# Performance work log

Hardware: AMD Instinct MI355X
Metric: run time of the kernel (lower is better)

The kernel has to match this reference:

```python
import jax, jax.numpy as jnp
import numpy as np
import math

B, T, C, H, D, R = 1, 2048, 2048, 16, 128, 64
W_LOCAL = 512
DELTA_I = 0.75
ROPE_BASE = 10000.0


def _rotate(x):
    # interleaved rotate-half, exactly as in the torch source
    x1, x2 = x[..., ::2], x[..., 1::2]
    return jnp.stack((-x2, x1), axis=-1).reshape(x.shape)


def _rope_tables(seq_len):
    inv_freq = 1.0 / (ROPE_BASE ** (jnp.arange(0, D, 2, dtype=jnp.float32) / D))
    t = jnp.arange(seq_len, dtype=jnp.float32)
    freqs = jnp.einsum('i,j->ij', t, inv_freq)          # [T, D/2]
    emb = jnp.concatenate((freqs, freqs), axis=-1)      # [T, D] (half-layout, as in source)
    return jnp.cos(emb)[None, None], jnp.sin(emb)[None, None]


def setup_inputs() -> dict:
    key = jax.random.key(0)
    ks = jax.random.split(key, 8)
    s = 0.02
    return {
        'x': jax.random.normal(ks[0], (B, T, C), dtype=jnp.float32),
        'w_qkv': jax.random.normal(ks[1], (3 * C, C), dtype=jnp.float32) * s,
        'w_o': jax.random.normal(ks[2], (C, C), dtype=jnp.float32) * s,
        'pk': jax.random.normal(ks[3], (R, D), dtype=jnp.float32) * s,
        'pv': jax.random.normal(ks[4], (R, D), dtype=jnp.float32) * s,
        'uo': jax.random.normal(ks[5], (D, R), dtype=jnp.float32) * s,
        'info_w1': jax.random.normal(ks[6], (C // 4, C), dtype=jnp.float32) * s,
        'info_w2': jax.random.normal(ks[7], (1, C // 4), dtype=jnp.float32) * s,
    }


def reference(x, w_qkv, w_o, pk, pv, uo, info_w1, info_w2):
    Bx, Tx, Cx = x.shape
    scale = 1.0 / math.sqrt(D)

    qkv = x @ w_qkv.T                                   # [B,T,3C]
    q, k, v = jnp.split(qkv, 3, axis=-1)
    q = q.reshape(Bx, Tx, H, D).transpose(0, 2, 1, 3)   # [B,H,T,D]
    k = k.reshape(Bx, Tx, H, D).transpose(0, 2, 1, 3)
    v = v.reshape(Bx, Tx, H, D).transpose(0, 2, 1, 3)

    cos, sin = _rope_tables(Tx)
    q = q * cos + _rotate(q) * sin
    k = k * cos + _rotate(k) * sin

    # causal local-window attention (full [B,H,T,T] scores, as in source)
    w = min(W_LOCAL, Tx)
    idx = jnp.arange(Tx)
    rel = idx[None, :] - idx[:, None]                   # j - i
    local_mask = (rel > 0) | (rel < -(w - 1))           # True = masked
    scores = jnp.einsum('bhtd,bhsd->bhts', q, k) * scale
    scores = jnp.where(local_mask[None, None], -jnp.inf, scores)
    attn_local = jax.nn.softmax(scores, axis=-1)
    ctx_local = jnp.einsum('bhts,bhsd->bhtd', attn_local, v)

    # informational gate (no-grad path in source)
    h_info = jax.nn.gelu(x @ info_w1.T, approximate=False)
    info_score = jax.nn.sigmoid((h_info @ info_w2.T)[..., 0])   # [B,T]
    gate = (info_score > DELTA_I).astype(x.dtype)

    # low-rank global path (unmasked softmax over all tokens, as in source)
    k_r = jnp.einsum('bhsd,rd->bhsr', k, pk)
    v_r = jnp.einsum('bhsd,rd->bhsr', v, pv)
    q_r = jnp.einsum('bhtd,rd->bhtr', q, pk)
    scores_g = jnp.einsum('bhtr,bhsr->bhts', q_r, k_r) * (scale * D / R)
    attn_g = jax.nn.softmax(scores_g, axis=-1)
    ctx_g_r = jnp.einsum('bhts,bhsr->bhtr', attn_g, v_r)
    ctx_g = jnp.einsum('bhtr,dr->bhtd', ctx_g_r, uo)
    gate_q = gate[:, None, :, None]                     # [B,1,T,1]
    ctx = ctx_local + ctx_g * gate_q

    ctx = ctx.transpose(0, 2, 1, 3).reshape(Bx, Tx, Cx)
    return ctx @ w_o.T
```

## Files before the change

kernel.cpp:

```cpp
#include <hip/hip_runtime.h>
#include <hip/hip_bf16.h>
#include <math.h>

#define T_LEN 2048
#define C_DIM 2048
#define NH 16
#define HD 128
#define RANK 64
#define W_LOCAL 512
#define QKV_LD 6144
#define ROW_BF 12288
#define KB_OFF 4096
#define VB_OFF 8192
#define WO_OFF 6144
#define SCALE 0.08838834764831845f
#define SCALE_G 0.17677669529663687f
#define LOG1E4_OVER_64 0.14391156831212787f

typedef __bf16 bf16_t;
typedef __bf16 bf16x8 __attribute__((ext_vector_type(8)));
typedef __bf16 bf16x4 __attribute__((ext_vector_type(4)));
typedef float f32x4 __attribute__((ext_vector_type(4)));

__device__ __forceinline__ void async_copy16(const bf16_t* g, bf16_t* l) {
    __builtin_amdgcn_global_load_lds(
        (const __attribute__((address_space(1))) unsigned int*)g,
        (__attribute__((address_space(3))) unsigned int*)l, 16, 0, 0);
}

__global__ __launch_bounds__(256)
void prep_kernel(const float* __restrict__ x, bf16_t* __restrict__ xb,
                 bf16_t* __restrict__ xlo,
                 const float* __restrict__ w1, bf16_t* __restrict__ w1hi,
                 bf16_t* __restrict__ w1lo,
                 const float* __restrict__ w_qkv, bf16_t* __restrict__ wqb,
                 float* __restrict__ tab) {
    const int bid = blockIdx.x;
    const int tid = threadIdx.x;
    if (bid < 2560) {
        const float* in;
        bf16_t *hi, *lo;
        int idx;
        if (bid < 2048) { in = x; hi = xb; lo = xlo; idx = bid * 256 + tid; }
        else            { in = w1; hi = w1hi; lo = w1lo; idx = (bid - 2048) * 256 + tid; }
        const float* p = in + (size_t)idx * 8;
        float4 v0 = *(const float4*)p;
        float4 v1 = *(const float4*)(p + 4);
        float v[8] = {v0.x, v0.y, v0.z, v0.w, v1.x, v1.y, v1.z, v1.w};
        bf16x8 h, l;
#pragma unroll
        for (int i = 0; i < 8; ++i) {
            bf16_t hb = (bf16_t)v[i];
            h[i] = hb;
            l[i] = (bf16_t)(v[i] - (float)hb);
        }
        *(bf16x8*)(hi + (size_t)idx * 8) = h;
        *(bf16x8*)(lo + (size_t)idx * 8) = l;
    } else if (bid < 8704) {
        int idx = (bid - 2560) * 256 + tid;
        const float* p = w_qkv + (size_t)idx * 8;
        float4 v0 = *(const float4*)p;
        float4 v1 = *(const float4*)(p + 4);
        bf16x8 o;
        o[0] = (bf16_t)v0.x; o[1] = (bf16_t)v0.y; o[2] = (bf16_t)v0.z; o[3] = (bf16_t)v0.w;
        o[4] = (bf16_t)v1.x; o[5] = (bf16_t)v1.y; o[6] = (bf16_t)v1.z; o[7] = (bf16_t)v1.w;
        *(bf16x8*)(wqb + (size_t)idx * 8) = o;
    } else {
        int idx = (bid - 8704) * 256 + tid;
        int t = idx >> 6, j = idx & 63;
        float inv = expf(-(float)j * LOG1E4_OVER_64);
        float s, c;
        sincosf((float)t * inv, &s, &c);
        tab[t * 128 + j] = c;
        tab[t * 128 + 64 + j] = s;
    }
}

#define NTK 32

#define STG_A(bb, ktile) do {                                                  \
    _Pragma("unroll")                                                          \
    for (int c_ = 0; c_ < 4; ++c_)                                             \
        async_copy16(gA + (size_t)(c_ * 32) * 2048 + (ktile) * 64,             \
                     &lds[bb][0][(c_ * 32 + rS) * 64 + dS]);                   \
} while (0)

#define STG_B(bb, ktile) do {                                                  \
    _Pragma("unroll")                                                          \
    for (int c_ = 0; c_ < 4; ++c_)                                             \
        async_copy16(gB + (size_t)(c_ * 32) * 2048 + (ktile) * 64,             \
                     &lds[bb][1][(c_ * 32 + rS) * 64 + dS]);                   \
} while (0)

#define RD_A(bb, m, k) (*(const bf16x8*)&lds[bb][0][(wr * 64 + (m) * 16 + l16) * 64 + (((k) * 4 + quad) ^ xsw) * 8])
#define RD_B(bb, n, k) (*(const bf16x8*)&lds[bb][1][(wc * 64 + (n) * 16 + l16) * 64 + (((k) * 4 + quad) ^ xsw) * 8])

__global__ __launch_bounds__(256, 2)
void gemm_qkv_rope(const bf16_t* __restrict__ A, const bf16_t* __restrict__ B,
                   float* __restrict__ qkv, bf16_t* __restrict__ qkv_bf,
                   const float* __restrict__ tab, const float* __restrict__ w_o) {
    const int bid = blockIdx.x;
    const int tid = threadIdx.x;
    if (bid >= 768) {
        int row = bid - 768;
        int c = tid * 8;
        const float* p = w_o + (size_t)row * 2048 + c;
        float4 v0 = *(const float4*)p;
        float4 v1 = *(const float4*)(p + 4);
        bf16x8 o;
        o[0] = (bf16_t)v0.x; o[1] = (bf16_t)v0.y; o[2] = (bf16_t)v0.z; o[3] = (bf16_t)v0.w;
        o[4] = (bf16_t)v1.x; o[5] = (bf16_t)v1.y; o[6] = (bf16_t)v1.z; o[7] = (bf16_t)v1.w;
        *(bf16x8*)(qkv_bf + (size_t)row * ROW_BF + WO_OFF + c) = o;
        return;
    }

    __shared__ __align__(16) bf16_t lds[2][2][128 * 64];

    const int xcd = bid & 7, idx = bid >> 3;
    const int bn_ = xcd * 6 + (idx >> 4);
    const int bm_ = idx & 15;
    const int wave = tid >> 6, lane = tid & 63;
    const int quad = lane >> 4, l16 = lane & 15;
    const int wr = wave >> 1, wc = wave & 1;
    const int xsw = l16 & 7;

    const int rS = tid >> 3;
    const int cS = ((tid & 7) ^ (rS & 7)) * 8;
    const int dS = (tid & 7) * 8;
    const bf16_t* gA = A + (size_t)(bm_ * 128 + rS) * 2048 + cS;
    const bf16_t* gB = B + (size_t)(bn_ * 128 + rS) * 2048 + cS;

    f32x4 acc[4][4];
#pragma unroll
    for (int i = 0; i < 4; ++i)
#pragma unroll
        for (int j = 0; j < 4; ++j) acc[i][j] = (f32x4){0.f, 0.f, 0.f, 0.f};

    STG_A(0, 0); STG_B(0, 0);
    STG_A(1, 1); STG_B(1, 1);
    asm volatile("s_waitcnt vmcnt(8)" ::: "memory");
    __builtin_amdgcn_s_barrier();

    for (int kt = 0; kt < NTK; ++kt) {
        const int b = kt & 1;
        bf16x8 af[4][2], bfr[4][2];
#pragma unroll
        for (int m = 0; m < 4; ++m) { af[m][0] = RD_A(b, m, 0); af[m][1] = RD_A(b, m, 1); }
#pragma unroll
        for (int n = 0; n < 4; ++n) { bfr[n][0] = RD_B(b, n, 0); bfr[n][1] = RD_B(b, n, 1); }
        asm volatile("s_waitcnt lgkmcnt(0)" ::: "memory");
        __builtin_amdgcn_s_barrier();

        __builtin_amdgcn_s_setprio(1);
#pragma unroll
        for (int m = 0; m < 4; ++m)
#pragma unroll
            for (int n = 0; n < 4; ++n)
                acc[m][n] = __builtin_amdgcn_mfma_f32_16x16x32_bf16(af[m][0], bfr[n][0], acc[m][n], 0, 0, 0);
        __builtin_amdgcn_s_setprio(0);
        if (kt + 2 < NTK) STG_A(b, kt + 2);

        __builtin_amdgcn_s_setprio(1);
#pragma unroll
        for (int m = 0; m < 4; ++m)
#pragma unroll
            for (int n = 0; n < 4; ++n)
                acc[m][n] = __builtin_amdgcn_mfma_f32_16x16x32_bf16(af[m][1], bfr[n][1], acc[m][n], 0, 0, 0);
        __builtin_amdgcn_s_setprio(0);
        if (kt + 2 < NTK) STG_B(b, kt + 2);

        if (kt < NTK - 2) { asm volatile("s_waitcnt vmcnt(8)" ::: "memory"); }
        else              { asm volatile("s_waitcnt vmcnt(0)" ::: "memory"); }
        __builtin_amdgcn_s_barrier();
    }

    const int colbase = bn_ * 128 + wc * 64;
    const int region = colbase >> 11;
    const int rowbase = bm_ * 128 + wr * 64;
    const bool odd = (l16 & 1);

    if (region == 2) {
#pragma unroll
        for (int mt = 0; mt < 4; ++mt)
#pragma unroll
            for (int r = 0; r < 4; ++r) {
                int t = rowbase + mt * 16 + quad * 4 + r;
                bf16_t* brow = qkv_bf + (size_t)t * ROW_BF + VB_OFF + (colbase - 4096);
#pragma unroll
                for (int nt = 0; nt < 4; ++nt)
                    brow[nt * 16 + l16] = (bf16_t)acc[mt][nt][r];
            }
    } else {
#pragma unroll
        for (int mt = 0; mt < 4; ++mt)
#pragma unroll
            for (int r = 0; r < 4; ++r) {
                int t = rowbase + mt * 16 + quad * 4 + r;
                const float* trow = tab + t * 128;
#pragma unroll
                for (int nt = 0; nt < 4; ++nt) {
                    float v = acc[mt][nt][r];
                    float vp = __shfl_xor(v, 1);
                    int col = colbase + nt * 16 + l16;
                    int j = col & 63;
                    float c = trow[j], s = trow[64 + j];
                    float y = odd ? (v * c + vp * s) : (v * c - vp * s);
                    if (region == 0)
                        qkv[(size_t)t * QKV_LD + col] = y;
                    else
                        qkv_bf[(size_t)t * ROW_BF + KB_OFF + (col - 2048)] = (bf16_t)y;
                }
            }
    }
}

#define STG_A2(bb, ktile) do {                                                 \
    _Pragma("unroll")                                                          \
    for (int c_ = 0; c_ < 4; ++c_)                                             \
        async_copy16(gA + (size_t)(c_ * 32) * 2048 + (ktile) * 64,             \
                     &lds[bb][0][(c_ * 32 + rS) * 64 + dS]);                   \
} while (0)

#define STG_B2(bb, ktile) do {                                                 \
    _Pragma("unroll")                                                          \
    for (int c_ = 0; c_ < 4; ++c_)                                             \
        async_copy16(gB + (size_t)(c_ * 32) * ROW_BF + (ktile) * 64,           \
                     &lds[bb][1][(c_ * 32 + rS) * 64 + dS]);                   \
} while (0)

__global__ __launch_bounds__(256, 2)
void gemm_ctx_wo(const bf16_t* __restrict__ A, const bf16_t* __restrict__ Bov,
                 float* __restrict__ C) {
    __shared__ __align__(16) bf16_t lds[2][2][128 * 64];

    const int bid = blockIdx.x;
    const int xcd = bid & 7, idx = bid >> 3;
    const int bn_ = xcd * 2 + (idx >> 4);
    const int bm_ = idx & 15;
    const int tid = threadIdx.x;
    const int wave = tid >> 6, lane = tid & 63;
    const int quad = lane >> 4, l16 = lane & 15;
    const int wr = wave >> 1, wc = wave & 1;
    const int xsw = l16 & 7;

    const int rS = tid >> 3;
    const int cS = ((tid & 7) ^ (rS & 7)) * 8;
    const int dS = (tid & 7) * 8;
    const bf16_t* gA = A + (size_t)(bm_ * 128 + rS) * 2048 + cS;
    const bf16_t* gB = Bov + (size_t)(bn_ * 128 + rS) * ROW_BF + cS;

    f32x4 acc[4][4];
#pragma unroll
    for (int i = 0; i < 4; ++i)
#pragma unroll
        for (int j = 0; j < 4; ++j) acc[i][j] = (f32x4){0.f, 0.f, 0.f, 0.f};

    STG_A2(0, 0); STG_B2(0, 0);
    STG_A2(1, 1); STG_B2(1, 1);
    asm volatile("s_waitcnt vmcnt(8)" ::: "memory");
    __builtin_amdgcn_s_barrier();

    for (int kt = 0; kt < NTK; ++kt) {
        const int b = kt & 1;
        bf16x8 af[4][2], bfr[4][2];
#pragma unroll
        for (int m = 0; m < 4; ++m) { af[m][0] = RD_A(b, m, 0); af[m][1] = RD_A(b, m, 1); }
#pragma unroll
        for (int n = 0; n < 4; ++n) { bfr[n][0] = RD_B(b, n, 0); bfr[n][1] = RD_B(b, n, 1); }
        asm volatile("s_waitcnt lgkmcnt(0)" ::: "memory");
        __builtin_amdgcn_s_barrier();

        __builtin_amdgcn_s_setprio(1);
#pragma unroll
        for (int m = 0; m < 4; ++m)
#pragma unroll
            for (int n = 0; n < 4; ++n)
                acc[m][n] = __builtin_amdgcn_mfma_f32_16x16x32_bf16(af[m][0], bfr[n][0], acc[m][n], 0, 0, 0);
        __builtin_amdgcn_s_setprio(0);
        if (kt + 2 < NTK) STG_A2(b, kt + 2);

        __builtin_amdgcn_s_setprio(1);
#pragma unroll
        for (int m = 0; m < 4; ++m)
#pragma unroll
            for (int n = 0; n < 4; ++n)
                acc[m][n] = __builtin_amdgcn_mfma_f32_16x16x32_bf16(af[m][1], bfr[n][1], acc[m][n], 0, 0, 0);
        __builtin_amdgcn_s_setprio(0);
        if (kt + 2 < NTK) STG_B2(b, kt + 2);

        if (kt < NTK - 2) { asm volatile("s_waitcnt vmcnt(8)" ::: "memory"); }
        else              { asm volatile("s_waitcnt vmcnt(0)" ::: "memory"); }
        __builtin_amdgcn_s_barrier();
    }

    const int colbase = bn_ * 128 + wc * 64;
    const int rowbase = bm_ * 128 + wr * 64;
#pragma unroll
    for (int mt = 0; mt < 4; ++mt)
#pragma unroll
        for (int r = 0; r < 4; ++r) {
            int row = rowbase + mt * 16 + quad * 4 + r;
            float* crow = C + (size_t)row * 2048 + colbase;
#pragma unroll
            for (int nt = 0; nt < 4; ++nt)
                crow[nt * 16 + l16] = acc[mt][nt][r];
        }
}

#define GBK 32

__global__ __launch_bounds__(256)
void info_gemm_mfma(const bf16_t* __restrict__ Ahi, const bf16_t* __restrict__ Alo,
                    const bf16_t* __restrict__ Bhi, const bf16_t* __restrict__ Blo,
                    float* __restrict__ Cpart) {
    __shared__ bf16_t Ah[128 * GBK];
    __shared__ bf16_t Al[128 * GBK];
    __shared__ bf16_t Bh[128 * GBK];
    __shared__ bf16_t Bl[128 * GBK];
    const int tid = threadIdx.x;
    const int wave = tid >> 6, lane = tid & 63;
    const int quad = lane >> 4, l16 = lane & 15;
    const int bm = blockIdx.y * 128, bn = blockIdx.x * 128;
    const int ks = blockIdx.z;
    const int wm = (wave >> 1) * 64, wn = (wave & 1) * 64;
    const int lrow = lane >> 2;
    const int lkb = (lane & 3) * 8;
    const int kbeg = ks * 512;

    f32x4 acc[4][4];
#pragma unroll
    for (int i = 0; i < 4; ++i)
#pragma unroll
        for (int j = 0; j < 4; ++j) acc[i][j] = (f32x4){0.f, 0.f, 0.f, 0.f};

    const size_t aoff = (size_t)(bm + wave * 16 + lrow) * 2048 + lkb + kbeg;
    const size_t boff = (size_t)(bn + wave * 16 + lrow) * 2048 + lkb + kbeg;
    bf16_t* lAh = &Ah[(wave * 16 + lrow) * GBK + lkb];
    bf16_t* lAl = &Al[(wave * 16 + lrow) * GBK + lkb];
    bf16_t* lBh = &Bh[(wave * 16 + lrow) * GBK + lkb];
    bf16_t* lBl = &Bl[(wave * 16 + lrow) * GBK + lkb];

    for (int k0 = 0; k0 < 512; k0 += GBK) {
        __syncthreads();
        async_copy16(Ahi + aoff + k0, lAh);
        async_copy16(Ahi + aoff + (size_t)64 * 2048 + k0, lAh + 64 * GBK);
        async_copy16(Alo + aoff + k0, lAl);
        async_copy16(Alo + aoff + (size_t)64 * 2048 + k0, lAl + 64 * GBK);
        async_copy16(Bhi + boff + k0, lBh);
        async_copy16(Bhi + boff + (size_t)64 * 2048 + k0, lBh + 64 * GBK);
        async_copy16(Blo + boff + k0, lBl);
        async_copy16(Blo + boff + (size_t)64 * 2048 + k0, lBl + 64 * GBK);
        __syncthreads();

        bf16x8 ah[4], al[4], bh[4], bl[4];
#pragma unroll
        for (int mt = 0; mt < 4; ++mt) {
            ah[mt] = *(const bf16x8*)&Ah[(wm + mt * 16 + l16) * GBK + quad * 8];
            al[mt] = *(const bf16x8*)&Al[(wm + mt * 16 + l16) * GBK + quad * 8];
        }
#pragma unroll
        for (int nt = 0; nt < 4; ++nt) {
            bh[nt] = *(const bf16x8*)&Bh[(wn + nt * 16 + l16) * GBK + quad * 8];
            bl[nt] = *(const bf16x8*)&Bl[(wn + nt * 16 + l16) * GBK + quad * 8];
        }
#pragma unroll
        for (int mt = 0; mt < 4; ++mt)
#pragma unroll
            for (int nt = 0; nt < 4; ++nt) {
                acc[mt][nt] = __builtin_amdgcn_mfma_f32_16x16x32_bf16(ah[mt], bh[nt], acc[mt][nt], 0, 0, 0);
                acc[mt][nt] = __builtin_amdgcn_mfma_f32_16x16x32_bf16(ah[mt], bl[nt], acc[mt][nt], 0, 0, 0);
                acc[mt][nt] = __builtin_amdgcn_mfma_f32_16x16x32_bf16(al[mt], bh[nt], acc[mt][nt], 0, 0, 0);
            }
    }

    float* cp = Cpart + (size_t)ks * 2048 * 512;
#pragma unroll
    for (int mt = 0; mt < 4; ++mt)
#pragma unroll
        for (int r = 0; r < 4; ++r) {
            int row = bm + wm + mt * 16 + quad * 4 + r;
            float* crow = cp + (size_t)row * 512 + bn + wn;
#pragma unroll
            for (int nt = 0; nt < 4; ++nt)
                crow[nt * 16 + l16] = acc[mt][nt][r];
        }
}

__device__ __forceinline__ float gelu_exact(float v) {
    return 0.5f * v * (1.0f + erff(v * 0.70710678118654752f));
}

__global__ __launch_bounds__(64)
void info_gate_kernel(const float* __restrict__ Cpart, const float* __restrict__ w2,
                      float* __restrict__ gate) {
    const int t = blockIdx.x;
    const int lane = threadIdx.x;
    const float* p0 = Cpart + (size_t)t * 512;
    float s = 0.f;
#pragma unroll
    for (int i = lane; i < 512; i += 64) {
        float v = ((p0[i] + p0[i + 1048576]) + p0[i + 2097152]) + p0[i + 3145728];
        s += gelu_exact(v) * w2[i];
    }
#pragma unroll
    for (int off = 32; off > 0; off >>= 1) s += __shfl_down(s, off);
    if (lane == 0) {
        float sig = 1.f / (1.f + expf(-s));
        gate[t] = (sig > 0.75f) ? 1.f : 0.f;
    }
}

#define KV_LD 136

__global__ __launch_bounds__(256)
void kvr_mfma_kernel(const float* __restrict__ qkv, const bf16_t* __restrict__ qkv_bf,
                     const float* __restrict__ pk, const float* __restrict__ pv,
                     float* __restrict__ kr, float* __restrict__ vr,
                     bf16_t* __restrict__ qr) {
    __shared__ bf16_t Kt[64 * KV_LD];
    __shared__ bf16_t Vt[64 * KV_LD];
    __shared__ bf16_t Qt[64 * KV_LD];
    __shared__ bf16_t Pk[64 * KV_LD];
    __shared__ bf16_t Pv[64 * KV_LD];

    const int h = blockIdx.y;
    const int s0 = blockIdx.x * 64;
    const int tid = threadIdx.x;
    const int wave = tid >> 6, lane = tid & 63;
    const int quad = lane >> 4, l16 = lane & 15;

#pragma unroll
    for (int i = 0; i < 4; ++i) {
        int gid = i * 256 + tid;
        int row = gid >> 4, ch = (gid & 15) << 3;
        const bf16_t* rb = qkv_bf + (size_t)(s0 + row) * ROW_BF + h * HD + ch;
        *(bf16x8*)&Kt[row * KV_LD + ch] = *(const bf16x8*)(rb + KB_OFF);
        *(bf16x8*)&Vt[row * KV_LD + ch] = *(const bf16x8*)(rb + VB_OFF);
    }
#pragma unroll
    for (int i = 0; i < 8; ++i) {
        int gid = i * 256 + tid;
        int row = gid >> 5, c = (gid & 31) << 2;
        float4 vq = *(const float4*)(qkv + (size_t)(s0 + row) * QKV_LD + h * HD + c);
        bf16x4 pq;
        pq[0] = (bf16_t)vq.x; pq[1] = (bf16_t)vq.y; pq[2] = (bf16_t)vq.z; pq[3] = (bf16_t)vq.w;
        *(bf16x4*)&Qt[row * KV_LD + c] = pq;
        float4 wk = *(const float4*)(pk + (size_t)row * HD + c);
        float4 wv = *(const float4*)(pv + (size_t)row * HD + c);
        bf16x4 qk4, qv4;
        qk4[0] = (bf16_t)wk.x; qk4[1] = (bf16_t)wk.y; qk4[2] = (bf16_t)wk.z; qk4[3] = (bf16_t)wk.w;
        qv4[0] = (bf16_t)wv.x; qv4[1] = (bf16_t)wv.y; qv4[2] = (bf16_t)wv.z; qv4[3] = (bf16_t)wv.w;
        *(bf16x4*)&Pk[row * KV_LD + c] = qk4;
        *(bf16x4*)&Pv[row * KV_LD + c] = qv4;
    }
    __syncthreads();

    f32x4 ak[4], av[4], aq[4];
#pragma unroll
    for (int nt = 0; nt < 4; ++nt) {
        ak[nt] = (f32x4){0.f, 0.f, 0.f, 0.f};
        av[nt] = (f32x4){0.f, 0.f, 0.f, 0.f};
        aq[nt] = (f32x4){0.f, 0.f, 0.f, 0.f};
    }

#pragma unroll
    for (int ks = 0; ks < 4; ++ks) {
        const int ao = (wave * 16 + l16) * KV_LD + ks * 32 + quad * 8;
        bf16x8 a_k = *(const bf16x8*)&Kt[ao];
        bf16x8 a_v = *(const bf16x8*)&Vt[ao];
        bf16x8 a_q = *(const bf16x8*)&Qt[ao];
#pragma unroll
        for (int nt = 0; nt < 4; ++nt) {
            const int bo = (nt * 16 + l16) * KV_LD + ks * 32 + quad * 8;
            bf16x8 bk = *(const bf16x8*)&Pk[bo];
            bf16x8 bv = *(const bf16x8*)&Pv[bo];
            ak[nt] = __builtin_amdgcn_mfma_f32_16x16x32_bf16(a_k, bk, ak[nt], 0, 0, 0);
            av[nt] = __builtin_amdgcn_mfma_f32_16x16x32_bf16(a_v, bv, av[nt], 0, 0, 0);
            aq[nt] = __builtin_amdgcn_mfma_f32_16x16x32_bf16(a_q, bk, aq[nt], 0, 0, 0);
        }
    }

#pragma unroll
    for (int nt = 0; nt < 4; ++nt)
#pragma unroll
        for (int r = 0; r < 4; ++r) {
            int s = s0 + wave * 16 + quad * 4 + r;
            size_t idx = ((size_t)h * T_LEN + s) * RANK + nt * 16 + l16;
            kr[idx] = ak[nt][r];
            vr[idx] = av[nt][r];
            qr[idx] = (bf16_t)aq[nt][r];
        }
}

#define QTI 64
#define KTI 64
#define QS_LD 136
#define VT_LD 68
#define PS_LD 72

__global__ __launch_bounds__(256)
void local_attn_kernel(const float* __restrict__ qkv, const bf16_t* __restrict__ qkv_bf,
                       bf16_t* __restrict__ cxb) {
    __shared__ bf16_t Qs[QTI * QS_LD];
    __shared__ bf16_t Ks[KTI * HD];
    __shared__ bf16_t Vt[HD * VT_LD];
    __shared__ bf16_t Ps[4][16 * PS_LD];

    const int h = blockIdx.y;
    const int t0 = blockIdx.x * QTI;
    const int tid = threadIdx.x;
    const int wave = tid >> 6, lane = tid & 63;
    const int quad = lane >> 4, l16 = lane & 15;

#pragma unroll
    for (int i = 0; i < 8; ++i) {
        int gid = i * 256 + tid;
        int row = gid >> 5, c4 = (gid & 31) << 2;
        const float4 v = *(const float4*)(qkv + (size_t)(t0 + row) * QKV_LD + h * HD + c4);
        bf16x4 p;
        p[0] = (bf16_t)(v.x * SCALE); p[1] = (bf16_t)(v.y * SCALE);
        p[2] = (bf16_t)(v.z * SCALE); p[3] = (bf16_t)(v.w * SCALE);
        *(bf16x4*)&Qs[row * QS_LD + c4] = p;
    }

    f32x4 o[8];
#pragma unroll
    for (int d8 = 0; d8 < 8; ++d8) o[d8] = (f32x4){0.f, 0.f, 0.f, 0.f};
    float m_i[4] = {-1e30f, -1e30f, -1e30f, -1e30f};
    float l_i[4] = {0.f, 0.f, 0.f, 0.f};

    __syncthreads();

    for (int kt = 0; kt < 9; ++kt) {
        const int sbase = t0 - 512 + kt * KTI;
        if (sbase < 0) continue;
        __syncthreads();
#pragma unroll
        for (int i = 0; i < 4; ++i) {
            int s = i * 256 + tid;
            int row = s >> 4, ch = s & 15;
            int gch = ch ^ (row & 7);
            const bf16_t* src = qkv_bf + (size_t)(sbase + row) * ROW_BF + KB_OFF + h * HD + gch * 8;
            async_copy16(src, &Ks[s * 8]);
        }
#pragma unroll
        for (int i = 0; i < 8; ++i) {
            int gid = i * 256 + tid;
            int row = gid >> 5, c4 = (gid & 31) << 2;
            bf16x4 vv = *(const bf16x4*)(qkv_bf + (size_t)(sbase + row) * ROW_BF + VB_OFF + h * HD + c4);
            Vt[(c4 + 0) * VT_LD + row] = vv[0];
            Vt[(c4 + 1) * VT_LD + row] = vv[1];
            Vt[(c4 + 2) * VT_LD + row] = vv[2];
            Vt[(c4 + 3) * VT_LD + row] = vv[3];
        }
        __syncthreads();

        f32x4 sacc[4];
#pragma unroll
        for (int nt = 0; nt < 4; ++nt) sacc[nt] = (f32x4){0.f, 0.f, 0.f, 0.f};
#pragma unroll
        for (int ks = 0; ks < 4; ++ks) {
            bf16x8 a = *(const bf16x8*)&Qs[(wave * 16 + l16) * QS_LD + ks * 32 + quad * 8];
#pragma unroll
            for (int nt = 0; nt < 4; ++nt) {
                int r = nt * 16 + l16;
                int ch = (ks * 4 + quad) ^ (r & 7);
                bf16x8 b = *(const bf16x8*)&Ks[r * HD + ch * 8];
                sacc[nt] = __builtin_amdgcn_mfma_f32_16x16x32_bf16(a, b, sacc[nt], 0, 0, 0);
            }
        }

        if (kt == 0 || kt == 8) {
#pragma unroll
            for (int nt = 0; nt < 4; ++nt) {
                int s_g = sbase + nt * 16 + l16;
#pragma unroll
                for (int r = 0; r < 4; ++r) {
                    int t_g = t0 + wave * 16 + quad * 4 + r;
                    bool valid = (s_g <= t_g) && (s_g + W_LOCAL > t_g);
                    if (!valid) sacc[nt][r] = -1e30f;
                }
            }
        }

#pragma unroll
        for (int r = 0; r < 4; ++r) {
            float mx = fmaxf(fmaxf(sacc[0][r], sacc[1][r]), fmaxf(sacc[2][r], sacc[3][r]));
            mx = fmaxf(mx, __shfl_xor(mx, 1));
            mx = fmaxf(mx, __shfl_xor(mx, 2));
            mx = fmaxf(mx, __shfl_xor(mx, 4));
            mx = fmaxf(mx, __shfl_xor(mx, 8));
            float mnew = fmaxf(m_i[r], mx);
            float alpha = __expf(m_i[r] - mnew);
            m_i[r] = mnew;
            float rs = 0.f;
#pragma unroll
            for (int nt = 0; nt < 4; ++nt) {
                float p = __expf(sacc[nt][r] - mnew);
                sacc[nt][r] = p;
                rs += p;
            }
            rs += __shfl_xor(rs, 1);
            rs += __shfl_xor(rs, 2);
            rs += __shfl_xor(rs, 4);
            rs += __shfl_xor(rs, 8);
            l_i[r] = l_i[r] * alpha + rs;
#pragma unroll
            for (int d8 = 0; d8 < 8; ++d8) o[d8][r] *= alpha;
        }

#pragma unroll
        for (int r = 0; r < 4; ++r)
#pragma unroll
            for (int nt = 0; nt < 4; ++nt)
                Ps[wave][(quad * 4 + r) * PS_LD + nt * 16 + l16] = (bf16_t)sacc[nt][r];

#pragma unroll
        for (int ks2 = 0; ks2 < 2; ++ks2) {
            bf16x8 a = *(const bf16x8*)&Ps[wave][l16 * PS_LD + ks2 * 32 + quad * 8];
#pragma unroll
            for (int d8 = 0; d8 < 8; ++d8) {
                const bf16_t* vb = &Vt[(d8 * 16 + l16) * VT_LD + ks2 * 32 + quad * 8];
                bf16x4 b0 = *(const bf16x4*)vb;
                bf16x4 b1 = *(const bf16x4*)(vb + 4);
                bf16x8 b;
                b[0] = b0[0]; b[1] = b0[1]; b[2] = b0[2]; b[3] = b0[3];
                b[4] = b1[0]; b[5] = b1[1]; b[6] = b1[2]; b[7] = b1[3];
                o[d8] = __builtin_amdgcn_mfma_f32_16x16x32_bf16(a, b, o[d8], 0, 0, 0);
            }
        }
    }

#pragma unroll
    for (int r = 0; r < 4; ++r) {
        float inv = 1.0f / l_i[r];
        size_t rowoff = (size_t)(t0 + wave * 16 + quad * 4 + r) * 2048 + h * HD;
#pragma unroll
        for (int d8 = 0; d8 < 8; ++d8)
            cxb[rowoff + d8 * 16 + l16] = (bf16_t)(o[d8][r] * inv);
    }
}

__device__ __forceinline__ float block_reduce_max512(float v, float* red, int tid) {
    red[tid] = v; __syncthreads();
    for (int s = 256; s > 0; s >>= 1) {
        if (tid < s) red[tid] = fmaxf(red[tid], red[tid + s]);
        __syncthreads();
    }
    float r = red[0]; __syncthreads();
    return r;
}
__device__ __forceinline__ float block_reduce_sum512(float v, float* red, int tid) {
    red[tid] = v; __syncthreads();
    for (int s = 256; s > 0; s >>= 1) {
        if (tid < s) red[tid] = red[tid] + red[tid + s];
        __syncthreads();
    }
    float r = red[0]; __syncthreads();
    return r;
}

__global__ __launch_bounds__(512)
void global_attn_kernel(bf16_t* __restrict__ cxb, const float* __restrict__ kr,
                        const float* __restrict__ vr, const bf16_t* __restrict__ qr,
                        const float* __restrict__ uo, const float* __restrict__ gate) {
    const int t = blockIdx.x, h = blockIdx.y;
    if (gate[t] <= 0.5f) return;

    __shared__ float qrs[64];
    __shared__ float red[512];
    __shared__ float cgr[64];
    __shared__ float sg[2048];
    const int tid = threadIdx.x;

    if (tid < 64) qrs[tid] = (float)qr[((size_t)h * T_LEN + t) * RANK + tid];
    __syncthreads();

    const float* krh = kr + (size_t)h * T_LEN * RANK;
    const float* vrh = vr + (size_t)h * T_LEN * RANK;
    float lmax = -INFINITY;
    for (int s = tid; s < T_LEN; s += 512) {
        const float* krr = krh + (size_t)s * RANK;
        float acc = 0.f;
#pragma unroll
        for (int r = 0; r < RANK; r += 4) {
            float4 k4 = *(const float4*)(krr + r);
            acc += qrs[r] * k4.x + qrs[r + 1] * k4.y + qrs[r + 2] * k4.z + qrs[r + 3] * k4.w;
        }
        float sc = acc * SCALE_G;
        sg[s] = sc;
        lmax = fmaxf(lmax, sc);
    }
    float gmx = block_reduce_max512(lmax, red, tid);
    float lsum = 0.f;
    for (int s = tid; s < T_LEN; s += 512) {
        float pp = expf(sg[s] - gmx);
        sg[s] = pp;
        lsum += pp;
    }
    float gsum = block_reduce_sum512(lsum, red, tid);

    {
        const int r = tid & 63, part = tid >> 6;
        float pacc = 0.f;
        for (int s = part; s < T_LEN; s += 8) pacc += sg[s] * vrh[(size_t)s * RANK + r];
        red[tid] = pacc;
        __syncthreads();
        if (tid < 64) {
            float c = 0.f;
#pragma unroll
            for (int pp = 0; pp < 8; ++pp) c += red[pp * 64 + tid];
            cgr[tid] = c / gsum;
        }
        __syncthreads();
    }

    if (tid < 128) {
        float cg = 0.f;
#pragma unroll
        for (int r = 0; r < RANK; ++r) cg += cgr[r] * uo[tid * RANK + r];
        size_t off = (size_t)t * 2048 + h * HD + tid;
        cxb[off] = (bf16_t)((float)cxb[off] + cg);
    }
}

extern "C" void kernel_launch(void* const* d_in, const int* in_sizes, int n_in,
                              void* d_out, int out_size, void* d_ws, size_t ws_size,
                              hipStream_t stream) {
    const float* x     = (const float*)d_in[0];
    const float* w_qkv = (const float*)d_in[1];
    const float* w_o   = (const float*)d_in[2];
    const float* pk    = (const float*)d_in[3];
    const float* pv    = (const float*)d_in[4];
    const float* uo    = (const float*)d_in[5];
    const float* w1    = (const float*)d_in[6];
    const float* w2    = (const float*)d_in[7];
    float* out = (float*)d_out;

    float* ws = (float*)d_ws;
    float* qkv   = ws;
    float* hinfo = qkv + (size_t)12582912;
    float* gatep = hinfo + (size_t)1048576;
    bf16_t* xb   = (bf16_t*)(gatep + 2048);
    float* wqbf  = gatep + 2048 + 2097152;
    bf16_t* wqb  = (bf16_t*)wqbf;
    float* krp   = wqbf;
    float* vrp   = wqbf + (size_t)2097152;
    float* tabp  = hinfo;
    bf16_t* qrp  = (bf16_t*)hinfo;
    bf16_t* cxb  = xb;
    bf16_t* qkvb = (bf16_t*)qkv;
    bf16_t* wob  = qkvb + WO_OFF;
    float* ipart  = qkv;
    bf16_t* xlo   = (bf16_t*)(qkv + 4194304);
    bf16_t* w1hi  = (bf16_t*)(qkv + 6291456);
    bf16_t* w1lo  = (bf16_t*)(qkv + 6815744);

    prep_kernel<<<9216, 256, 0, stream>>>(x, xb, xlo, w1, w1hi, w1lo, w_qkv, wqb, tabp);
    info_gemm_mfma<<<dim3(4, 16, 4), 256, 0, stream>>>(xb, xlo, w1hi, w1lo, ipart);
    info_gate_kernel<<<T_LEN, 64, 0, stream>>>(ipart, w2, gatep);
    gemm_qkv_rope<<<2816, 256, 0, stream>>>(xb, wqb, qkv, qkvb, tabp, w_o);
    kvr_mfma_kernel<<<dim3(T_LEN / 64, NH), 256, 0, stream>>>(qkv, qkvb, pk, pv, krp, vrp, qrp);
    local_attn_kernel<<<dim3(T_LEN / QTI, NH), 256, 0, stream>>>(qkv, qkvb, cxb);
    global_attn_kernel<<<dim3(T_LEN, NH), 512, 0, stream>>>(cxb, krp, vrp, qrp, uo, gatep);
    gemm_ctx_wo<<<256, 256, 0, stream>>>(cxb, wob, out);
}
```

Before: 343.4 us.

## Store Q as bf16 and pre-transposed V from QKV GEMM for async attention loads

The QKV GEMM epilogue now writes Q in bf16 into the shared bf16 buffer instead of fp32. It also transposes V through LDS and writes a per-head transposed V into the output buffer used as scratch. The local attention kernel then loads Q, K and V with swizzled 16-byte async copies, replacing scalar transposing stores, and applies the softmax scale after QK^T. The goal is to cut global traffic and the scattered LDS writes in attention. The cost is Q rounded to bf16 before scaling and an extra transpose step in the GEMM epilogue.

Result: faster. 307.7 us (-10.4%).

```diff
diff --git a/kernel.cpp b/kernel.cpp
--- a/kernel.cpp
+++ b/kernel.cpp
@@ -97,7 +97,7 @@
 
 __global__ __launch_bounds__(256, 2)
 void gemm_qkv_rope(const bf16_t* __restrict__ A, const bf16_t* __restrict__ B,
-                   float* __restrict__ qkv, bf16_t* __restrict__ qkv_bf,
+                   bf16_t* __restrict__ qkv_bf, bf16_t* __restrict__ vt,
                    const float* __restrict__ tab, const float* __restrict__ w_o) {
     const int bid = blockIdx.x;
     const int tid = threadIdx.x;
@@ -175,7 +175,7 @@
     }
 
     const int colbase = bn_ * 128 + wc * 64;
-    const int region = colbase >> 11;
+    const int region = (bn_ * 128) >> 11;
     const int rowbase = bm_ * 128 + wr * 64;
     const bool odd = (l16 & 1);
 
@@ -190,6 +190,26 @@
                 for (int nt = 0; nt < 4; ++nt)
                     brow[nt * 16 + l16] = (bf16_t)acc[mt][nt][r];
             }
+        bf16_t* Tl = (bf16_t*)lds;
+#pragma unroll
+        for (int mt = 0; mt < 4; ++mt)
+#pragma unroll
+            for (int r = 0; r < 4; ++r) {
+                int rloc = wr * 64 + mt * 16 + quad * 4 + r;
+#pragma unroll
+                for (int nt = 0; nt < 4; ++nt) {
+                    int cloc = wc * 64 + nt * 16 + l16;
+                    Tl[cloc * 136 + rloc] = (bf16_t)acc[mt][nt][r];
+                }
+            }
+        __syncthreads();
+        const int hh = bn_ - 32;
+        const int d = tid >> 1, th = (tid & 1) * 64;
+        bf16_t* dst = vt + ((size_t)(hh * 128 + d)) * 2048 + bm_ * 128 + th;
+        const bf16_t* srcT = Tl + d * 136 + th;
+#pragma unroll
+        for (int j = 0; j < 8; ++j)
+            *(bf16x8*)(dst + j * 8) = *(const bf16x8*)(srcT + j * 8);
     } else {
 #pragma unroll
         for (int mt = 0; mt < 4; ++mt)
@@ -205,10 +225,7 @@
                     int j = col & 63;
                     float c = trow[j], s = trow[64 + j];
                     float y = odd ? (v * c + vp * s) : (v * c - vp * s);
-                    if (region == 0)
-                        qkv[(size_t)t * QKV_LD + col] = y;
-                    else
-                        qkv_bf[(size_t)t * ROW_BF + KB_OFF + (col - 2048)] = (bf16_t)y;
+                    qkv_bf[(size_t)t * ROW_BF + (region == 0 ? col : col + 2048)] = (bf16_t)y;
                 }
             }
     }
@@ -413,7 +430,7 @@
 #define KV_LD 136
 
 __global__ __launch_bounds__(256)
-void kvr_mfma_kernel(const float* __restrict__ qkv, const bf16_t* __restrict__ qkv_bf,
+void kvr_mfma_kernel(const bf16_t* __restrict__ qkv_bf,
                      const float* __restrict__ pk, const float* __restrict__ pv,
                      float* __restrict__ kr, float* __restrict__ vr,
                      bf16_t* __restrict__ qr) {
@@ -434,6 +451,7 @@
         int gid = i * 256 + tid;
         int row = gid >> 4, ch = (gid & 15) << 3;
         const bf16_t* rb = qkv_bf + (size_t)(s0 + row) * ROW_BF + h * HD + ch;
+        *(bf16x8*)&Qt[row * KV_LD + ch] = *(const bf16x8*)(rb);
         *(bf16x8*)&Kt[row * KV_LD + ch] = *(const bf16x8*)(rb + KB_OFF);
         *(bf16x8*)&Vt[row * KV_LD + ch] = *(const bf16x8*)(rb + VB_OFF);
     }
@@ -441,10 +459,6 @@
     for (int i = 0; i < 8; ++i) {
         int gid = i * 256 + tid;
         int row = gid >> 5, c = (gid & 31) << 2;
-        float4 vq = *(const float4*)(qkv + (size_t)(s0 + row) * QKV_LD + h * HD + c);
-        bf16x4 pq;
-        pq[0] = (bf16_t)vq.x; pq[1] = (bf16_t)vq.y; pq[2] = (bf16_t)vq.z; pq[3] = (bf16_t)vq.w;
-        *(bf16x4*)&Qt[row * KV_LD + c] = pq;
         float4 wk = *(const float4*)(pk + (size_t)row * HD + c);
         float4 wv = *(const float4*)(pv + (size_t)row * HD + c);
         bf16x4 qk4, qv4;
@@ -494,16 +508,14 @@
 
 #define QTI 64
 #define KTI 64
-#define QS_LD 136
-#define VT_LD 68
 #define PS_LD 72
 
 __global__ __launch_bounds__(256)
-void local_attn_kernel(const float* __restrict__ qkv, const bf16_t* __restrict__ qkv_bf,
+void local_attn_kernel(const bf16_t* __restrict__ qkv_bf, const bf16_t* __restrict__ vt,
                        bf16_t* __restrict__ cxb) {
-    __shared__ bf16_t Qs[QTI * QS_LD];
-    __shared__ bf16_t Ks[KTI * HD];
-    __shared__ bf16_t Vt[HD * VT_LD];
+    __shared__ __align__(16) bf16_t Qs[QTI * 128];
+    __shared__ __align__(16) bf16_t Ks[KTI * 128];
+    __shared__ __align__(16) bf16_t Vts[128 * KTI];
     __shared__ bf16_t Ps[4][16 * PS_LD];
 
     const int h = blockIdx.y;
@@ -511,16 +523,16 @@
     const int tid = threadIdx.x;
     const int wave = tid >> 6, lane = tid & 63;
     const int quad = lane >> 4, l16 = lane & 15;
-
-#pragma unroll
-    for (int i = 0; i < 8; ++i) {
-        int gid = i * 256 + tid;
-        int row = gid >> 5, c4 = (gid & 31) << 2;
-        const float4 v = *(const float4*)(qkv + (size_t)(t0 + row) * QKV_LD + h * HD + c4);
-        bf16x4 p;
-        p[0] = (bf16_t)(v.x * SCALE); p[1] = (bf16_t)(v.y * SCALE);
-        p[2] = (bf16_t)(v.z * SCALE); p[3] = (bf16_t)(v.w * SCALE);
-        *(bf16x4*)&Qs[row * QS_LD + c4] = p;
+    const int xsw = l16 & 7;
+
+    const bf16_t* vth = vt + (size_t)h * 128 * 2048;
+
+#pragma unroll
+    for (int i = 0; i < 4; ++i) {
+        int c = i * 256 + tid;
+        int row = c >> 4, pc = c & 15;
+        int lc = pc ^ (row & 7);
+        async_copy16(qkv_bf + (size_t)(t0 + row) * ROW_BF + h * HD + lc * 8, &Qs[c * 8]);
     }
 
     f32x4 o[8];
@@ -537,21 +549,18 @@
         __syncthreads();
 #pragma unroll
         for (int i = 0; i < 4; ++i) {
-            int s = i * 256 + tid;
-            int row = s >> 4, ch = s & 15;
-            int gch = ch ^ (row & 7);
-            const bf16_t* src = qkv_bf + (size_t)(sbase + row) * ROW_BF + KB_OFF + h * HD + gch * 8;
-            async_copy16(src, &Ks[s * 8]);
-        }
-#pragma unroll
-        for (int i = 0; i < 8; ++i) {
-            int gid = i * 256 + tid;
-            int row = gid >> 5, c4 = (gid & 31) << 2;
-            bf16x4 vv = *(const bf16x4*)(qkv_bf + (size_t)(sbase + row) * ROW_BF + VB_OFF + h * HD + c4);
-            Vt[(c4 + 0) * VT_LD + row] = vv[0];
-            Vt[(c4 + 1) * VT_LD + row] = vv[1];
-            Vt[(c4 + 2) * VT_LD + row] = vv[2];
-            Vt[(c4 + 3) * VT_LD + row] = vv[3];
+            int c = i * 256 + tid;
+            int row = c >> 4, pc = c & 15;
+            int lc = pc ^ (row & 7);
+            async_copy16(qkv_bf + (size_t)(sbase + row) * ROW_BF + KB_OFF + h * HD + lc * 8,
+                         &Ks[c * 8]);
+        }
+#pragma unroll
+        for (int i = 0; i < 4; ++i) {
+            int c = i * 256 + tid;
+            int row = c >> 3, pc = c & 7;
+            int lc = pc ^ (row & 7);
+            async_copy16(vth + (size_t)row * 2048 + sbase + lc * 8, &Vts[c * 8]);
         }
         __syncthreads();
 
@@ -560,15 +569,18 @@
         for (int nt = 0; nt < 4; ++nt) sacc[nt] = (f32x4){0.f, 0.f, 0.f, 0.f};
 #pragma unroll
         for (int ks = 0; ks < 4; ++ks) {
-            bf16x8 a = *(const bf16x8*)&Qs[(wave * 16 + l16) * QS_LD + ks * 32 + quad * 8];
+            bf16x8 a = *(const bf16x8*)&Qs[(wave * 16 + l16) * 128 + (((ks * 4 + quad) ^ xsw)) * 8];
 #pragma unroll
             for (int nt = 0; nt < 4; ++nt) {
-                int r = nt * 16 + l16;
-                int ch = (ks * 4 + quad) ^ (r & 7);
-                bf16x8 b = *(const bf16x8*)&Ks[r * HD + ch * 8];
+                bf16x8 b = *(const bf16x8*)&Ks[(nt * 16 + l16) * 128 + (((ks * 4 + quad) ^ xsw)) * 8];
                 sacc[nt] = __builtin_amdgcn_mfma_f32_16x16x32_bf16(a, b, sacc[nt], 0, 0, 0);
             }
         }
+
+#pragma unroll
+        for (int nt = 0; nt < 4; ++nt)
+#pragma unroll
+            for (int r = 0; r < 4; ++r) sacc[nt][r] *= SCALE;
 
         if (kt == 0 || kt == 8) {
 #pragma unroll
@@ -620,12 +632,8 @@
             bf16x8 a = *(const bf16x8*)&Ps[wave][l16 * PS_LD + ks2 * 32 + quad * 8];
 #pragma unroll
             for (int d8 = 0; d8 < 8; ++d8) {
-                const bf16_t* vb = &Vt[(d8 * 16 + l16) * VT_LD + ks2 * 32 + quad * 8];
-                bf16x4 b0 = *(const bf16x4*)vb;
-                bf16x4 b1 = *(const bf16x4*)(vb + 4);
-                bf16x8 b;
-                b[0] = b0[0]; b[1] = b0[1]; b[2] = b0[2]; b[3] = b0[3];
-                b[4] = b1[0]; b[5] = b1[1]; b[6] = b1[2]; b[7] = b1[3];
+                int rw = d8 * 16 + l16;
+                bf16x8 b = *(const bf16x8*)&Vts[rw * 64 + (((ks2 * 4 + quad) ^ xsw)) * 8];
                 o[d8] = __builtin_amdgcn_mfma_f32_16x16x32_bf16(a, b, o[d8], 0, 0, 0);
             }
         }
@@ -751,6 +759,7 @@
     bf16_t* cxb  = xb;
     bf16_t* qkvb = (bf16_t*)qkv;
     bf16_t* wob  = qkvb + WO_OFF;
+    bf16_t* vtp  = (bf16_t*)d_out;
     float* ipart  = qkv;
     bf16_t* xlo   = (bf16_t*)(qkv + 4194304);
     bf16_t* w1hi  = (bf16_t*)(qkv + 6291456);
@@ -759,9 +768,9 @@
     prep_kernel<<<9216, 256, 0, stream>>>(x, xb, xlo, w1, w1hi, w1lo, w_qkv, wqb, tabp);
     info_gemm_mfma<<<dim3(4, 16, 4), 256, 0, stream>>>(xb, xlo, w1hi, w1lo, ipart);
     info_gate_kernel<<<T_LEN, 64, 0, stream>>>(ipart, w2, gatep);
-    gemm_qkv_rope<<<2816, 256, 0, stream>>>(xb, wqb, qkv, qkvb, tabp, w_o);
-    kvr_mfma_kernel<<<dim3(T_LEN / 64, NH), 256, 0, stream>>>(qkv, qkvb, pk, pv, krp, vrp, qrp);
-    local_attn_kernel<<<dim3(T_LEN / QTI, NH), 256, 0, stream>>>(qkv, qkvb, cxb);
+    gemm_qkv_rope<<<2816, 256, 0, stream>>>(xb, wqb, qkvb, vtp, tabp, w_o);
+    kvr_mfma_kernel<<<dim3(T_LEN / 64, NH), 256, 0, stream>>>(qkvb, pk, pv, krp, vrp, qrp);
+    local_attn_kernel<<<dim3(T_LEN / QTI, NH), 256, 0, stream>>>(qkvb, vtp, cxb);
     global_attn_kernel<<<dim3(T_LEN, NH), 512, 0, stream>>>(cxb, krp, vrp, qrp, uo, gatep);
     gemm_ctx_wo<<<256, 256, 0, stream>>>(cxb, wob, out);
 }
```
